# Performance work log

Hardware: AMD Instinct MI355X
Metric: run time of the kernel (lower is better)

Reference implementation:

```python
import jax, jax.numpy as jnp
import numpy as np

N = 20000      # num nodes
E = 320000     # num edges (before self loops)
DIN = 128      # in_channels
DH = 128       # hidden channels
C = 40         # num classes


def setup_inputs() -> dict:
    key = jax.random.key(0)
    ks = jax.random.split(key, 16)
    s_in = 1.0 / np.sqrt(DIN)
    s_h = 1.0 / np.sqrt(DH)
    s_a = 1.0 / np.sqrt(2 * DH)
    return {
        "x": jax.random.normal(ks[0], (N, DIN), jnp.float32),
        "edge_index": jax.random.randint(ks[1], (2, E), 0, N),
        "norm": jax.random.uniform(ks[2], (E + N,), jnp.float32),  # Jaccard sims in [0,1]
        # layer 1 params
        "W1": jax.random.uniform(ks[3], (DIN, DH), jnp.float32, -s_in, s_in),
        "aW1": jax.random.uniform(ks[4], (2 * DH, 1), jnp.float32, -s_a, s_a),
        "ab1": jax.random.uniform(ks[5], (1,), jnp.float32, -s_a, s_a),
        "alpha1": jnp.array([0.5], jnp.float32),
        "b1": jnp.zeros((DH,), jnp.float32),
        # layer 2 params
        "W2": jax.random.uniform(ks[6], (DH, DH), jnp.float32, -s_h, s_h),
        "aW2": jax.random.uniform(ks[7], (2 * DH, 1), jnp.float32, -s_a, s_a),
        "ab2": jax.random.uniform(ks[8], (1,), jnp.float32, -s_a, s_a),
        "alpha2": jnp.array([0.5], jnp.float32),
        "b2": jnp.zeros((DH,), jnp.float32),
        # output head
        "Wout": jax.random.uniform(ks[9], (DH, C), jnp.float32, -s_h, s_h),
        "bout": jax.random.uniform(ks[10], (C,), jnp.float32, -s_h, s_h),
    }


def _gat_layer(x, src, dst, norm, W, aW, ab, alpha, bias):
    n = x.shape[0]
    h = x @ W                              # [N, DH]
    s = h[src]                             # gathered source feats [E', DH]
    t = h[dst]                             # gathered target feats [E', DH]
    # attention logit per edge -> exp(leaky_relu(.))
    e = jnp.exp(jax.nn.leaky_relu(jnp.concatenate([s, t], axis=-1) @ aW + ab,
                                  negative_slope=0.2))          # [E', 1]
    e_sum = jax.ops.segment_sum(e, dst, num_segments=n)         # softmax denom per dst node
    a = e / e_sum[dst]
    s_sim = jnp.exp(norm)[:, None]                               # [E', 1]
    s_sum = jax.ops.segment_sum(s_sim, src, num_segments=n)     # note: summed over SRC (as in original)
    sw = s_sim / s_sum[dst]                                      # but indexed by DST (as in original)
    al = jnp.clip(alpha, 1e-4, 0.9999)
    w = al * a + (1.0 - al) * sw                                 # blended edge weight [E', 1]
    out = jax.ops.segment_max(w * s, dst, num_segments=n)        # aggr='max' propagate
    return out + bias


def reference(x, edge_index, norm, W1, aW1, ab1, alpha1, b1,
              W2, aW2, ab2, alpha2, b2, Wout, bout):
    n = x.shape[0]
    loops = jnp.arange(n, dtype=edge_index.dtype)
    src = jnp.concatenate([edge_index[0], loops])   # add_self_loops
    dst = jnp.concatenate([edge_index[1], loops])
    h = jax.nn.relu(_gat_layer(x, src, dst, norm, W1, aW1, ab1, alpha1, b1))
    h = jax.nn.relu(_gat_layer(h, src, dst, norm, W2, aW2, ab2, alpha2, b2))
    return jax.nn.log_softmax(h @ Wout + bout, axis=-1)
```

## Files before the change

kernel.cpp:

```cpp
#include <hip/hip_runtime.h>
#include <math.h>

#define DHID 128
#define NCLS 40
#define ELLW 64

typedef unsigned int   u32;
typedef unsigned short u16;
using short8 = __attribute__((ext_vector_type(8))) short;
using f32x4  = __attribute__((ext_vector_type(4))) float;

__device__ __forceinline__ u16 f2bf(float f) {
  u32 u = __float_as_uint(f);
  return (u16)((u + 0x7FFFu + ((u >> 16) & 1u)) >> 16);
}
__device__ __forceinline__ float bf_lo(u32 p) { return __uint_as_float(p << 16); }
__device__ __forceinline__ float bf_hi(u32 p) { return __uint_as_float(p & 0xFFFF0000u); }

__global__ __launch_bounds__(256) void prep_kernel(
    const float* __restrict__ x, const float* __restrict__ W1,
    const float* __restrict__ W2, u16* __restrict__ xbf,
    u16* __restrict__ Wp1, u16* __restrict__ Wp2,
    int* __restrict__ counts, float* __restrict__ ssum,
    int* __restrict__ ovf_cnt, int N) {
  int gi = blockIdx.x * 256 + threadIdx.x;
  int Ncvt = N * 16;
  if (gi < Ncvt) {
    int base = gi * 8;
    float4 v0 = *reinterpret_cast<const float4*>(x + base);
    float4 v1 = *reinterpret_cast<const float4*>(x + base + 4);
    uint4 o;
    o.x = (u32)f2bf(v0.x) | ((u32)f2bf(v0.y) << 16);
    o.y = (u32)f2bf(v0.z) | ((u32)f2bf(v0.w) << 16);
    o.z = (u32)f2bf(v1.x) | ((u32)f2bf(v1.y) << 16);
    o.w = (u32)f2bf(v1.z) | ((u32)f2bf(v1.w) << 16);
    *reinterpret_cast<uint4*>(xbf + base) = o;
    return;
  }
  gi -= Ncvt;
  if (gi < N) { counts[gi] = 0; ssum[gi] = 0.f; return; }
  gi -= N;
  if (gi < 32768) {
    int layer = gi >> 14, q = gi & 16383;
    int j = q & 7, l = (q >> 3) & 63, kt = (q >> 9) & 3, ct = q >> 11;
    int k = kt * 32 + (l >> 4) * 8 + j;
    int col = ct * 16 + (l & 15);
    const float* Wsrc = layer ? W2 : W1;
    u16* Wdst = layer ? Wp2 : Wp1;
    Wdst[q] = f2bf(Wsrc[k * DHID + col]);
    return;
  }
  gi -= 32768;
  if (gi == 0) *ovf_cnt = 0;
}

__device__ __forceinline__ void mfma_gemm_block(
    float* Cl, float* P, const u16* __restrict__ Xbf,
    const u16* __restrict__ Wp, const float* __restrict__ aW,
    u16* __restrict__ Hout, float* __restrict__ elo, float* __restrict__ ero,
    int n, int rowBase) {
  int t = threadIdx.x;
  int w = t >> 6, l = t & 63;
  int lr = l & 15, lh = l >> 4;
  f32x4 acc00 = {0.f,0.f,0.f,0.f}, acc01 = {0.f,0.f,0.f,0.f};
  f32x4 acc10 = {0.f,0.f,0.f,0.f}, acc11 = {0.f,0.f,0.f,0.f};
  int r0 = rowBase + lr;      if (r0 > n - 1) r0 = n - 1;
  int r1 = rowBase + 16 + lr; if (r1 > n - 1) r1 = n - 1;
  const u16* a0p = Xbf + (size_t)r0 * DHID;
  const u16* a1p = Xbf + (size_t)r1 * DHID;
  const u16* wb0 = Wp + ((size_t)(w * 2 + 0) * 4 * 64 + l) * 8;
  const u16* wb1 = Wp + ((size_t)(w * 2 + 1) * 4 * 64 + l) * 8;
#pragma unroll
  for (int kt = 0; kt < 4; ++kt) {
    int ko = kt * 32 + lh * 8;
    short8 fa0 = *reinterpret_cast<const short8*>(a0p + ko);
    short8 fa1 = *reinterpret_cast<const short8*>(a1p + ko);
    short8 fb0 = *reinterpret_cast<const short8*>(wb0 + kt * 64 * 8);
    short8 fb1 = *reinterpret_cast<const short8*>(wb1 + kt * 64 * 8);
    acc00 = __builtin_amdgcn_mfma_f32_16x16x32_bf16(fa0, fb0, acc00, 0, 0, 0);
    acc01 = __builtin_amdgcn_mfma_f32_16x16x32_bf16(fa0, fb1, acc01, 0, 0, 0);
    acc10 = __builtin_amdgcn_mfma_f32_16x16x32_bf16(fa1, fb0, acc10, 0, 0, 0);
    acc11 = __builtin_amdgcn_mfma_f32_16x16x32_bf16(fa1, fb1, acc11, 0, 0, 0);
  }
#pragma unroll
  for (int j = 0; j < 4; ++j) {
    Cl[(lh * 4 + j) * DHID + w * 32 + lr]           = acc00[j];
    Cl[(lh * 4 + j) * DHID + w * 32 + 16 + lr]      = acc01[j];
    Cl[(16 + lh * 4 + j) * DHID + w * 32 + lr]      = acc10[j];
    Cl[(16 + lh * 4 + j) * DHID + w * 32 + 16 + lr] = acc11[j];
  }
  __syncthreads();
  int r = t >> 3, cg2 = (t & 7) * 16;
  const float* crow = Cl + r * DHID + cg2;
  float pl = 0.f, pr = 0.f;
  int gr = rowBase + r;
#pragma unroll
  for (int q = 0; q < 16; ++q) {
    float v = crow[q];
    pl = fmaf(v, aW[cg2 + q], pl);
    pr = fmaf(v, aW[DHID + cg2 + q], pr);
  }
  if (gr < n) {
    uint4 o;
    o.x = (u32)f2bf(crow[0])  | ((u32)f2bf(crow[1])  << 16);
    o.y = (u32)f2bf(crow[2])  | ((u32)f2bf(crow[3])  << 16);
    o.z = (u32)f2bf(crow[4])  | ((u32)f2bf(crow[5])  << 16);
    o.w = (u32)f2bf(crow[6])  | ((u32)f2bf(crow[7])  << 16);
    *reinterpret_cast<uint4*>(Hout + (size_t)gr * DHID + cg2) = o;
    uint4 o2;
    o2.x = (u32)f2bf(crow[8])  | ((u32)f2bf(crow[9])  << 16);
    o2.y = (u32)f2bf(crow[10]) | ((u32)f2bf(crow[11]) << 16);
    o2.z = (u32)f2bf(crow[12]) | ((u32)f2bf(crow[13]) << 16);
    o2.w = (u32)f2bf(crow[14]) | ((u32)f2bf(crow[15]) << 16);
    *reinterpret_cast<uint4*>(Hout + (size_t)gr * DHID + cg2 + 8) = o2;
  }
  P[r * 16 + (t & 7) * 2 + 0] = pl;
  P[r * 16 + (t & 7) * 2 + 1] = pr;
  __syncthreads();
  if (t < 64) {
    int half = t >> 5, rr = t & 31;
    float s = 0.f;
#pragma unroll
    for (int cq = 0; cq < 8; ++cq) s += P[rr * 16 + cq * 2 + half];
    int g2 = rowBase + rr;
    if (g2 < n) { if (half) ero[g2] = s; else elo[g2] = s; }
  }
}

__global__ __launch_bounds__(256) void gemm1_build_kernel(
    const u16* __restrict__ Xbf, const u16* __restrict__ Wp,
    const float* __restrict__ aW, u16* __restrict__ H,
    float* __restrict__ el, float* __restrict__ er, int n, int gT,
    const int* __restrict__ ei, const float* __restrict__ norm,
    int* __restrict__ counts, float* __restrict__ ssum,
    uint2* __restrict__ ell, uint4* __restrict__ ovf,
    int* __restrict__ ovf_cnt, int E, int EP) {
  __shared__ float Cl[32 * DHID];
  __shared__ float P[32 * 16];
  if (blockIdx.x < gT) {
    mfma_gemm_block(Cl, P, Xbf, Wp, aW, H, el, er, n, blockIdx.x * 32);
  } else {
    int k = (blockIdx.x - gT) * 256 + threadIdx.x;
    if (k < EP) {
      int src, dst;
      if (k < E) { src = ei[k]; dst = ei[E + k]; }
      else       { src = dst = k - E; }
      float se = __expf(norm[k]);
      atomicAdd(&ssum[src], se);
      int slot = atomicAdd(&counts[dst], 1);
      if (slot < ELLW) {
        ell[(size_t)dst * ELLW + slot] =
            make_uint2((u32)src, __float_as_uint(se));
      } else {
        int o = atomicAdd(ovf_cnt, 1);
        ovf[o] = make_uint4((u32)dst, (u32)src, __float_as_uint(se), 0u);
      }
    }
  }
}

__global__ __launch_bounds__(256) void gemm_elr_kernel(
    const u16* __restrict__ Xbf, const u16* __restrict__ Wp,
    const float* __restrict__ aW, u16* __restrict__ H,
    float* __restrict__ el, float* __restrict__ er, int n) {
  __shared__ float Cl[32 * DHID];
  __shared__ float P[32 * 16];
  mfma_gemm_block(Cl, P, Xbf, Wp, aW, H, el, er, n, blockIdx.x * 32);
}

__device__ __forceinline__ void agg_node8(
    const u16* __restrict__ H, const int* __restrict__ counts,
    const uint2* __restrict__ ell, const uint4* __restrict__ ovf, int ovfN,
    const float* __restrict__ el, const float* __restrict__ ssum,
    float base, float al, int node, int lane, float a[8]) {
  int deg = counts[node];
  int dell = deg < ELLW ? deg : ELLW;
  const uint2* erow = ell + (size_t)node * ELLW;
  int src0 = 0; float sx0 = 0.f;
  if (lane < dell) {
    uint2 rec = erow[lane];
    src0 = (int)rec.x;
    sx0  = __uint_as_float(rec.y);
  }
  int qw = lane >> 4;
  const u16* Hf = H + ((lane & 15) << 3);
  int ei0 = qw, ei1 = 4 + qw;
  int ci0 = ei0 < dell ? ei0 : 0;
  int ci1 = ei1 < dell ? ei1 : 0;
  int ps0 = __shfl(src0, ci0);
  int ps1 = __shfl(src0, ci1);
  uint4 pr0 = *reinterpret_cast<const uint4*>(Hf + (size_t)ps0 * DHID);
  uint4 pr1 = *reinterpret_cast<const uint4*>(Hf + (size_t)ps1 * DHID);
  float e0 = 0.f;
  if (lane < dell) {
    float g = el[src0] + base;
    e0 = __expf(g > 0.f ? g : 0.2f * g);
  }
  float es = e0;
  if (ovfN > 0 && deg > ELLW) {
    for (int cb = 0; cb < ovfN; cb += 64) {
      int i = cb + lane;
      if (i < ovfN) {
        uint4 r = ovf[i];
        if ((int)r.x == node) {
          float g = el[(int)r.y] + base;
          es += __expf(g > 0.f ? g : 0.2f * g);
        }
      }
    }
  }
#pragma unroll
  for (int off = 32; off; off >>= 1) es += __shfl_xor(es, off);
  float invEs = al / es;
  float omaS  = (1.f - al) / ssum[node];
  float w0 = e0 * invEs + sx0 * omaS;
#pragma unroll
  for (int i = 0; i < 8; ++i) a[i] = -INFINITY;
  {
    float wA = __shfl(w0, ci0);
    float wB = __shfl(w0, ci1);
    if (ei0 < dell) {
      a[0] = fmaxf(a[0], wA * bf_lo(pr0.x)); a[1] = fmaxf(a[1], wA * bf_hi(pr0.x));
      a[2] = fmaxf(a[2], wA * bf_lo(pr0.y)); a[3] = fmaxf(a[3], wA * bf_hi(pr0.y));
      a[4] = fmaxf(a[4], wA * bf_lo(pr0.z)); a[5] = fmaxf(a[5], wA * bf_hi(pr0.z));
      a[6] = fmaxf(a[6], wA * bf_lo(pr0.w)); a[7] = fmaxf(a[7], wA * bf_hi(pr0.w));
    }
    if (ei1 < dell) {
      a[0] = fmaxf(a[0], wB * bf_lo(pr1.x)); a[1] = fmaxf(a[1], wB * bf_hi(pr1.x));
      a[2] = fmaxf(a[2], wB * bf_lo(pr1.y)); a[3] = fmaxf(a[3], wB * bf_hi(pr1.y));
      a[4] = fmaxf(a[4], wB * bf_lo(pr1.z)); a[5] = fmaxf(a[5], wB * bf_hi(pr1.z));
      a[6] = fmaxf(a[6], wB * bf_lo(pr1.w)); a[7] = fmaxf(a[7], wB * bf_hi(pr1.w));
    }
  }
  int j = 8;
  for (; j + 7 < dell; j += 8) {
    int ea = j + qw, eb = j + 4 + qw;
    int   sa = __shfl(src0, ea); float wa = __shfl(w0, ea);
    int   sb = __shfl(src0, eb); float wb = __shfl(w0, eb);
    uint4 ha = *reinterpret_cast<const uint4*>(Hf + (size_t)sa * DHID);
    uint4 hb = *reinterpret_cast<const uint4*>(Hf + (size_t)sb * DHID);
    a[0] = fmaxf(a[0], fmaxf(wa * bf_lo(ha.x), wb * bf_lo(hb.x)));
    a[1] = fmaxf(a[1], fmaxf(wa * bf_hi(ha.x), wb * bf_hi(hb.x)));
    a[2] = fmaxf(a[2], fmaxf(wa * bf_lo(ha.y), wb * bf_lo(hb.y)));
    a[3] = fmaxf(a[3], fmaxf(wa * bf_hi(ha.y), wb * bf_hi(hb.y)));
    a[4] = fmaxf(a[4], fmaxf(wa * bf_lo(ha.z), wb * bf_lo(hb.z)));
    a[5] = fmaxf(a[5], fmaxf(wa * bf_hi(ha.z), wb * bf_hi(hb.z)));
    a[6] = fmaxf(a[6], fmaxf(wa * bf_lo(ha.w), wb * bf_lo(hb.w)));
    a[7] = fmaxf(a[7], fmaxf(wa * bf_hi(ha.w), wb * bf_hi(hb.w)));
  }
  for (; j < dell; j += 4) {
    int e = j + qw;
    int ec = e < dell ? e : dell - 1;
    int   sa = __shfl(src0, ec); float wa = __shfl(w0, ec);
    if (e < dell) {
      uint4 ha = *reinterpret_cast<const uint4*>(Hf + (size_t)sa * DHID);
      a[0] = fmaxf(a[0], wa * bf_lo(ha.x));
      a[1] = fmaxf(a[1], wa * bf_hi(ha.x));
      a[2] = fmaxf(a[2], wa * bf_lo(ha.y));
      a[3] = fmaxf(a[3], wa * bf_hi(ha.y));
      a[4] = fmaxf(a[4], wa * bf_lo(ha.z));
      a[5] = fmaxf(a[5], wa * bf_hi(ha.z));
      a[6] = fmaxf(a[6], wa * bf_lo(ha.w));
      a[7] = fmaxf(a[7], wa * bf_hi(ha.w));
    }
  }
  if (ovfN > 0 && deg > ELLW) {
    for (int cb = 0; cb < ovfN; cb += 64) {
      int i = cb + lane;
      uint4 r = (i < ovfN) ? ovf[i] : make_uint4(0u, 0u, 0u, 0u);
      bool match = (i < ovfN) && ((int)r.x == node);
      int si = (int)r.y;
      float wi = 0.f;
      if (match) {
        float g = el[si] + base;
        wi = __expf(g > 0.f ? g : 0.2f * g) * invEs +
             __uint_as_float(r.z) * omaS;
      }
      unsigned long long mask = __ballot(match);
      while (mask) {
        int jb = __ffsll(mask) - 1;
        mask &= mask - 1;
        int   sj = __shfl(si, jb);
        float wj = __shfl(wi, jb);
        uint4 h = *reinterpret_cast<const uint4*>(Hf + (size_t)sj * DHID);
        a[0] = fmaxf(a[0], wj * bf_lo(h.x)); a[1] = fmaxf(a[1], wj * bf_hi(h.x));
        a[2] = fmaxf(a[2], wj * bf_lo(h.y)); a[3] = fmaxf(a[3], wj * bf_hi(h.y));
        a[4] = fmaxf(a[4], wj * bf_lo(h.z)); a[5] = fmaxf(a[5], wj * bf_hi(h.z));
        a[6] = fmaxf(a[6], wj * bf_lo(h.w)); a[7] = fmaxf(a[7], wj * bf_hi(h.w));
      }
    }
  }
#pragma unroll
  for (int i = 0; i < 8; ++i) {
    a[i] = fmaxf(a[i], __shfl_xor(a[i], 16));
    a[i] = fmaxf(a[i], __shfl_xor(a[i], 32));
  }
}

__global__ __launch_bounds__(256, 8) void agg_kernel(
    const u16* __restrict__ H, const int* __restrict__ counts,
    const uint2* __restrict__ ell, const uint4* __restrict__ ovf,
    const int* __restrict__ ovf_cnt, const float* __restrict__ el,
    const float* __restrict__ er, const float* __restrict__ ssum,
    const float* __restrict__ ab, const float* __restrict__ alpha,
    const float* __restrict__ bias, u16* __restrict__ Y, int n) {
  int node = blockIdx.x * 4 + (threadIdx.x >> 6);
  int lane = threadIdx.x & 63;
  if (node >= n) return;
  int ovfN = *ovf_cnt;
  float al = fminf(fmaxf(alpha[0], 1e-4f), 0.9999f);
  float base = er[node] + ab[0];
  float a[8];
  agg_node8(H, counts, ell, ovf, ovfN, el, ssum, base, al, node, lane, a);
  if (lane < 16) {
    int fl = lane << 3;
    float v[8];
#pragma unroll
    for (int i = 0; i < 8; ++i) v[i] = fmaxf(a[i] + bias[fl + i], 0.f);
    uint4 o;
    o.x = (u32)f2bf(v[0]) | ((u32)f2bf(v[1]) << 16);
    o.y = (u32)f2bf(v[2]) | ((u32)f2bf(v[3]) << 16);
    o.z = (u32)f2bf(v[4]) | ((u32)f2bf(v[5]) << 16);
    o.w = (u32)f2bf(v[6]) | ((u32)f2bf(v[7]) << 16);
    *reinterpret_cast<uint4*>(Y + (size_t)node * DHID + fl) = o;
  }
}

__global__ __launch_bounds__(256, 7) void agg_head_kernel(
    const u16* __restrict__ H, const int* __restrict__ counts,
    const uint2* __restrict__ ell, const uint4* __restrict__ ovf,
    const int* __restrict__ ovf_cnt, const float* __restrict__ el,
    const float* __restrict__ er, const float* __restrict__ ssum,
    const float* __restrict__ ab, const float* __restrict__ alpha,
    const float* __restrict__ bias, const float* __restrict__ Wout,
    const float* __restrict__ bout, float* __restrict__ out, int n) {
  __shared__ float Wl[DHID * NCLS];
  __shared__ float hl[4][DHID];
  int t = threadIdx.x;
  for (int i = t; i < DHID * NCLS; i += 256) Wl[i] = Wout[i];
  int wv = t >> 6, lane = t & 63;
  int node = blockIdx.x * 4 + wv;
  if (node < n) {
    int ovfN = *ovf_cnt;
    float al = fminf(fmaxf(alpha[0], 1e-4f), 0.9999f);
    float base = er[node] + ab[0];
    float a[8];
    agg_node8(H, counts, ell, ovf, ovfN, el, ssum, base, al, node, lane, a);
    if (lane < 16) {
      int fl = lane << 3;
#pragma unroll
      for (int i = 0; i < 8; ++i)
        hl[wv][fl + i] = fmaxf(a[i] + bias[fl + i], 0.f);
    }
  }
  __syncthreads();
  if (node >= n) return;
  float z = -INFINITY;
  bool act = lane < NCLS;
  if (act) {
    z = bout[lane];
    const float* hr = hl[wv];
#pragma unroll 8
    for (int k = 0; k < DHID; ++k) z = fmaf(hr[k], Wl[k * NCLS + lane], z);
  }
  float m = z;
#pragma unroll
  for (int off = 32; off; off >>= 1) m = fmaxf(m, __shfl_xor(m, off));
  float p = act ? expf(z - m) : 0.f;
#pragma unroll
  for (int off = 32; off; off >>= 1) p += __shfl_xor(p, off);
  float ls = logf(p);
  if (act) out[(size_t)node * NCLS + lane] = z - m - ls;
}

extern "C" void kernel_launch(void* const* d_in, const int* in_sizes, int n_in,
                              void* d_out, int out_size, void* d_ws, size_t ws_size,
                              hipStream_t stream) {
  const float* x     = (const float*)d_in[0];
  const int*   ei    = (const int*)d_in[1];
  const float* norm  = (const float*)d_in[2];
  const float* W1    = (const float*)d_in[3];
  const float* aW1   = (const float*)d_in[4];
  const float* ab1   = (const float*)d_in[5];
  const float* alpha1= (const float*)d_in[6];
  const float* b1    = (const float*)d_in[7];
  const float* W2    = (const float*)d_in[8];
  const float* aW2   = (const float*)d_in[9];
  const float* ab2   = (const float*)d_in[10];
  const float* alpha2= (const float*)d_in[11];
  const float* b2    = (const float*)d_in[12];
  const float* Wout  = (const float*)d_in[13];
  const float* bout  = (const float*)d_in[14];
  float* out = (float*)d_out;

  const int N  = in_sizes[0] / DHID;
  const int E  = in_sizes[1] / 2;
  const int EP = E + N;

  char* ws = (char*)d_ws;
  size_t off = 0;
  auto alloc = [&](size_t bytes) -> void* {
    void* p = ws + off;
    off += (bytes + 255) & ~(size_t)255;
    return p;
  };
  int*   counts  = (int*)  alloc((size_t)N * 4);
  float* ssum    = (float*)alloc((size_t)N * 4);
  int*   ovf_cnt = (int*)  alloc(256);
  u16*   xbf     = (u16*)  alloc((size_t)N * DHID * 2);
  u16*   Wp1     = (u16*)  alloc(16384 * 2);
  u16*   Wp2     = (u16*)  alloc(16384 * 2);
  u16*   Hbf     = (u16*)  alloc((size_t)N * DHID * 2);
  u16*   Bbf     = (u16*)  alloc((size_t)N * DHID * 2);
  float* el      = (float*)alloc((size_t)N * 4);
  float* er      = (float*)alloc((size_t)N * 4);
  uint2* ell     = (uint2*)alloc((size_t)N * ELLW * 8);
  uint4* ovf     = (uint4*)alloc((size_t)EP * 16);

  const int gEdge = (EP + 255) / 256;
  const int gT    = (N + 31) / 32;
  const int gAgg  = (N + 3) / 4;
  const int prepWork = N * 16 + N + 32768 + 1;
  const int gPrep = (prepWork + 255) / 256;

  prep_kernel<<<gPrep, 256, 0, stream>>>(x, W1, W2, xbf, Wp1, Wp2,
                                         counts, ssum, ovf_cnt, N);
  gemm1_build_kernel<<<gT + gEdge, 256, 0, stream>>>(
      xbf, Wp1, aW1, Hbf, el, er, N, gT, ei, norm, counts, ssum, ell, ovf,
      ovf_cnt, E, EP);
  agg_kernel<<<gAgg, 256, 0, stream>>>(Hbf, counts, ell, ovf, ovf_cnt, el, er,
                                       ssum, ab1, alpha1, b1, Bbf, N);
  gemm_elr_kernel<<<gT, 256, 0, stream>>>(Bbf, Wp2, aW2, Hbf, el, er, N);
  agg_head_kernel<<<gAgg, 256, 0, stream>>>(Hbf, counts, ell, ovf, ovf_cnt,
                                            el, er, ssum, ab2, alpha2, b2,
                                            Wout, bout, out, N);
}
```

Measured before the change: 105.0 us.

## Process two destination nodes per wavefront in aggregation kernels

```diff
diff --git a/kernel.cpp b/kernel.cpp
--- a/kernel.cpp
+++ b/kernel.cpp
@@ -16,6 +16,16 @@
 }
 __device__ __forceinline__ float bf_lo(u32 p) { return __uint_as_float(p << 16); }
 __device__ __forceinline__ float bf_hi(u32 p) { return __uint_as_float(p & 0xFFFF0000u); }
+
+#define FMAX8(acc, wv, h)                                            \
+  acc[0] = fmaxf(acc[0], (wv) * bf_lo((h).x));                       \
+  acc[1] = fmaxf(acc[1], (wv) * bf_hi((h).x));                       \
+  acc[2] = fmaxf(acc[2], (wv) * bf_lo((h).y));                       \
+  acc[3] = fmaxf(acc[3], (wv) * bf_hi((h).y));                       \
+  acc[4] = fmaxf(acc[4], (wv) * bf_lo((h).z));                       \
+  acc[5] = fmaxf(acc[5], (wv) * bf_hi((h).z));                       \
+  acc[6] = fmaxf(acc[6], (wv) * bf_lo((h).w));                       \
+  acc[7] = fmaxf(acc[7], (wv) * bf_hi((h).w));
 
 __global__ __launch_bounds__(256) void prep_kernel(
     const float* __restrict__ x, const float* __restrict__ W1,
@@ -168,165 +178,198 @@
   mfma_gemm_block(Cl, P, Xbf, Wp, aW, H, el, er, n, blockIdx.x * 32);
 }
 
-__device__ __forceinline__ void agg_node8(
+__device__ __forceinline__ void agg_node8_dual(
     const u16* __restrict__ H, const int* __restrict__ counts,
     const uint2* __restrict__ ell, const uint4* __restrict__ ovf, int ovfN,
-    const float* __restrict__ el, const float* __restrict__ ssum,
-    float base, float al, int node, int lane, float a[8]) {
-  int deg = counts[node];
-  int dell = deg < ELLW ? deg : ELLW;
-  const uint2* erow = ell + (size_t)node * ELLW;
-  int src0 = 0; float sx0 = 0.f;
-  if (lane < dell) {
-    uint2 rec = erow[lane];
-    src0 = (int)rec.x;
-    sx0  = __uint_as_float(rec.y);
-  }
+    const float* __restrict__ el, const float* __restrict__ er,
+    const float* __restrict__ ssum, float abv, float al,
+    int nodeA, int nodeB, int n, int lane, float aA[8], float aB[8]) {
+  int nB = nodeB < n ? nodeB : nodeA;
+  int degA = counts[nodeA], degB = counts[nB];
+  int dellA = degA < ELLW ? degA : ELLW;
+  int dellB = degB < ELLW ? degB : ELLW;
+  const uint2* erowA = ell + (size_t)nodeA * ELLW;
+  const uint2* erowB = ell + (size_t)nB * ELLW;
+  int srcA = 0, srcB = 0; float sxA = 0.f, sxB = 0.f;
+  if (lane < dellA) { uint2 r = erowA[lane]; srcA = (int)r.x; sxA = __uint_as_float(r.y); }
+  if (lane < dellB) { uint2 r = erowB[lane]; srcB = (int)r.x; sxB = __uint_as_float(r.y); }
   int qw = lane >> 4;
   const u16* Hf = H + ((lane & 15) << 3);
   int ei0 = qw, ei1 = 4 + qw;
-  int ci0 = ei0 < dell ? ei0 : 0;
-  int ci1 = ei1 < dell ? ei1 : 0;
-  int ps0 = __shfl(src0, ci0);
-  int ps1 = __shfl(src0, ci1);
-  uint4 pr0 = *reinterpret_cast<const uint4*>(Hf + (size_t)ps0 * DHID);
-  uint4 pr1 = *reinterpret_cast<const uint4*>(Hf + (size_t)ps1 * DHID);
-  float e0 = 0.f;
-  if (lane < dell) {
-    float g = el[src0] + base;
-    e0 = __expf(g > 0.f ? g : 0.2f * g);
-  }
-  float es = e0;
-  if (ovfN > 0 && deg > ELLW) {
+  int cA0 = ei0 < dellA ? ei0 : 0, cA1 = ei1 < dellA ? ei1 : 0;
+  int cB0 = ei0 < dellB ? ei0 : 0, cB1 = ei1 < dellB ? ei1 : 0;
+  int pA0 = __shfl(srcA, cA0), pA1 = __shfl(srcA, cA1);
+  int pB0 = __shfl(srcB, cB0), pB1 = __shfl(srcB, cB1);
+  uint4 rA0 = *reinterpret_cast<const uint4*>(Hf + (size_t)pA0 * DHID);
+  uint4 rA1 = *reinterpret_cast<const uint4*>(Hf + (size_t)pA1 * DHID);
+  uint4 rB0 = *reinterpret_cast<const uint4*>(Hf + (size_t)pB0 * DHID);
+  uint4 rB1 = *reinterpret_cast<const uint4*>(Hf + (size_t)pB1 * DHID);
+  float baseA = er[nodeA] + abv, baseB = er[nB] + abv;
+  float eA = 0.f, eB = 0.f;
+  if (lane < dellA) { float g = el[srcA] + baseA; eA = __expf(g > 0.f ? g : 0.2f * g); }
+  if (lane < dellB) { float g = el[srcB] + baseB; eB = __expf(g > 0.f ? g : 0.2f * g); }
+  float esA = eA, esB = eB;
+  if (ovfN > 0 && (degA > ELLW || degB > ELLW)) {
     for (int cb = 0; cb < ovfN; cb += 64) {
       int i = cb + lane;
       if (i < ovfN) {
         uint4 r = ovf[i];
-        if ((int)r.x == node) {
-          float g = el[(int)r.y] + base;
-          es += __expf(g > 0.f ? g : 0.2f * g);
-        }
-      }
-    }
-  }
-#pragma unroll
-  for (int off = 32; off; off >>= 1) es += __shfl_xor(es, off);
-  float invEs = al / es;
-  float omaS  = (1.f - al) / ssum[node];
-  float w0 = e0 * invEs + sx0 * omaS;
-#pragma unroll
-  for (int i = 0; i < 8; ++i) a[i] = -INFINITY;
+        if ((int)r.x == nodeA) { float g = el[(int)r.y] + baseA; esA += __expf(g > 0.f ? g : 0.2f * g); }
+        if ((int)r.x == nB)    { float g = el[(int)r.y] + baseB; esB += __expf(g > 0.f ? g : 0.2f * g); }
+      }
+    }
+  }
+#pragma unroll
+  for (int off = 32; off; off >>= 1) {
+    esA += __shfl_xor(esA, off);
+    esB += __shfl_xor(esB, off);
+  }
+  float invA = al / esA, invB = al / esB;
+  float omA = (1.f - al) / ssum[nodeA], omB = (1.f - al) / ssum[nB];
+  float w0A = eA * invA + sxA * omA;
+  float w0B = eB * invB + sxB * omB;
+#pragma unroll
+  for (int i = 0; i < 8; ++i) { aA[i] = -INFINITY; aB[i] = -INFINITY; }
   {
-    float wA = __shfl(w0, ci0);
-    float wB = __shfl(w0, ci1);
-    if (ei0 < dell) {
-      a[0] = fmaxf(a[0], wA * bf_lo(pr0.x)); a[1] = fmaxf(a[1], wA * bf_hi(pr0.x));
-      a[2] = fmaxf(a[2], wA * bf_lo(pr0.y)); a[3] = fmaxf(a[3], wA * bf_hi(pr0.y));
-      a[4] = fmaxf(a[4], wA * bf_lo(pr0.z)); a[5] = fmaxf(a[5], wA * bf_hi(pr0.z));
-      a[6] = fmaxf(a[6], wA * bf_lo(pr0.w)); a[7] = fmaxf(a[7], wA * bf_hi(pr0.w));
-    }
-    if (ei1 < dell) {
-      a[0] = fmaxf(a[0], wB * bf_lo(pr1.x)); a[1] = fmaxf(a[1], wB * bf_hi(pr1.x));
-      a[2] = fmaxf(a[2], wB * bf_lo(pr1.y)); a[3] = fmaxf(a[3], wB * bf_hi(pr1.y));
-      a[4] = fmaxf(a[4], wB * bf_lo(pr1.z)); a[5] = fmaxf(a[5], wB * bf_hi(pr1.z));
-      a[6] = fmaxf(a[6], wB * bf_lo(pr1.w)); a[7] = fmaxf(a[7], wB * bf_hi(pr1.w));
-    }
+    float wa = __shfl(w0A, cA0), wb = __shfl(w0A, cA1);
+    float wc = __shfl(w0B, cB0), wd = __shfl(w0B, cB1);
+    if (ei0 < dellA) { FMAX8(aA, wa, rA0) }
+    if (ei1 < dellA) { FMAX8(aA, wb, rA1) }
+    if (ei0 < dellB) { FMAX8(aB, wc, rB0) }
+    if (ei1 < dellB) { FMAX8(aB, wd, rB1) }
   }
   int j = 8;
-  for (; j + 7 < dell; j += 8) {
+  int dmin = dellA < dellB ? dellA : dellB;
+  for (; j + 7 < dmin; j += 8) {
     int ea = j + qw, eb = j + 4 + qw;
-    int   sa = __shfl(src0, ea); float wa = __shfl(w0, ea);
-    int   sb = __shfl(src0, eb); float wb = __shfl(w0, eb);
+    int sa = __shfl(srcA, ea); float wa = __shfl(w0A, ea);
+    int sb = __shfl(srcA, eb); float wb = __shfl(w0A, eb);
+    int sc = __shfl(srcB, ea); float wc = __shfl(w0B, ea);
+    int sd = __shfl(srcB, eb); float wd = __shfl(w0B, eb);
     uint4 ha = *reinterpret_cast<const uint4*>(Hf + (size_t)sa * DHID);
     uint4 hb = *reinterpret_cast<const uint4*>(Hf + (size_t)sb * DHID);
-    a[0] = fmaxf(a[0], fmaxf(wa * bf_lo(ha.x), wb * bf_lo(hb.x)));
-    a[1] = fmaxf(a[1], fmaxf(wa * bf_hi(ha.x), wb * bf_hi(hb.x)));
-    a[2] = fmaxf(a[2], fmaxf(wa * bf_lo(ha.y), wb * bf_lo(hb.y)));
-    a[3] = fmaxf(a[3], fmaxf(wa * bf_hi(ha.y), wb * bf_hi(hb.y)));
-    a[4] = fmaxf(a[4], fmaxf(wa * bf_lo(ha.z), wb * bf_lo(hb.z)));
-    a[5] = fmaxf(a[5], fmaxf(wa * bf_hi(ha.z), wb * bf_hi(hb.z)));
-    a[6] = fmaxf(a[6], fmaxf(wa * bf_lo(ha.w), wb * bf_lo(hb.w)));
-    a[7] = fmaxf(a[7], fmaxf(wa * bf_hi(ha.w), wb * bf_hi(hb.w)));
-  }
-  for (; j < dell; j += 4) {
-    int e = j + qw;
-    int ec = e < dell ? e : dell - 1;
-    int   sa = __shfl(src0, ec); float wa = __shfl(w0, ec);
-    if (e < dell) {
+    uint4 hc = *reinterpret_cast<const uint4*>(Hf + (size_t)sc * DHID);
+    uint4 hd = *reinterpret_cast<const uint4*>(Hf + (size_t)sd * DHID);
+    FMAX8(aA, wa, ha) FMAX8(aA, wb, hb)
+    FMAX8(aB, wc, hc) FMAX8(aB, wd, hd)
+  }
+  int jA = j, jB = j;
+  for (; jA + 7 < dellA; jA += 8) {
+    int ea = jA + qw, eb = jA + 4 + qw;
+    int sa = __shfl(srcA, ea); float wa = __shfl(w0A, ea);
+    int sb = __shfl(srcA, eb); float wb = __shfl(w0A, eb);
+    uint4 ha = *reinterpret_cast<const uint4*>(Hf + (size_t)sa * DHID);
+    uint4 hb = *reinterpret_cast<const uint4*>(Hf + (size_t)sb * DHID);
+    FMAX8(aA, wa, ha) FMAX8(aA, wb, hb)
+  }
+  for (; jA < dellA; jA += 4) {
+    int e = jA + qw;
+    int ec = e < dellA ? e : dellA - 1;
+    int sa = __shfl(srcA, ec); float wa = __shfl(w0A, ec);
+    if (e < dellA) {
       uint4 ha = *reinterpret_cast<const uint4*>(Hf + (size_t)sa * DHID);
-      a[0] = fmaxf(a[0], wa * bf_lo(ha.x));
-      a[1] = fmaxf(a[1], wa * bf_hi(ha.x));
-      a[2] = fmaxf(a[2], wa * bf_lo(ha.y));
-      a[3] = fmaxf(a[3], wa * bf_hi(ha.y));
-      a[4] = fmaxf(a[4], wa * bf_lo(ha.z));
-      a[5] = fmaxf(a[5], wa * bf_hi(ha.z));
-      a[6] = fmaxf(a[6], wa * bf_lo(ha.w));
-      a[7] = fmaxf(a[7], wa * bf_hi(ha.w));
-    }
-  }
-  if (ovfN > 0 && deg > ELLW) {
+      FMAX8(aA, wa, ha)
+    }
+  }
+  for (; jB + 7 < dellB; jB += 8) {
+    int ea = jB + qw, eb = jB + 4 + qw;
+    int sa = __shfl(srcB, ea); float wa = __shfl(w0B, ea);
+    int sb = __shfl(srcB, eb); float wb = __shfl(w0B, eb);
+    uint4 ha = *reinterpret_cast<const uint4*>(Hf + (size_t)sa * DHID);
+    uint4 hb = *reinterpret_cast<const uint4*>(Hf + (size_t)sb * DHID);
+    FMAX8(aB, wa, ha) FMAX8(aB, wb, hb)
+  }
+  for (; jB < dellB; jB += 4) {
+    int e = jB + qw;
+    int ec = e < dellB ? e : dellB - 1;
+    int sa = __shfl(srcB, ec); float wa = __shfl(w0B, ec);
+    if (e < dellB) {
+      uint4 ha = *reinterpret_cast<const uint4*>(Hf + (size_t)sa * DHID);
+      FMAX8(aB, wa, ha)
+    }
+  }
+  if (ovfN > 0 && (degA > ELLW || degB > ELLW)) {
     for (int cb = 0; cb < ovfN; cb += 64) {
       int i = cb + lane;
       uint4 r = (i < ovfN) ? ovf[i] : make_uint4(0u, 0u, 0u, 0u);
-      bool match = (i < ovfN) && ((int)r.x == node);
+      bool mA = (i < ovfN) && ((int)r.x == nodeA);
+      bool mB = (i < ovfN) && ((int)r.x == nB);
       int si = (int)r.y;
-      float wi = 0.f;
-      if (match) {
-        float g = el[si] + base;
-        wi = __expf(g > 0.f ? g : 0.2f * g) * invEs +
-             __uint_as_float(r.z) * omaS;
-      }
-      unsigned long long mask = __ballot(match);
+      float wiA = 0.f, wiB = 0.f;
+      if (mA) {
+        float g = el[si] + baseA;
+        wiA = __expf(g > 0.f ? g : 0.2f * g) * invA + __uint_as_float(r.z) * omA;
+      }
+      if (mB) {
+        float g = el[si] + baseB;
+        wiB = __expf(g > 0.f ? g : 0.2f * g) * invB + __uint_as_float(r.z) * omB;
+      }
+      unsigned long long mask = __ballot(mA);
       while (mask) {
-        int jb = __ffsll(mask) - 1;
-        mask &= mask - 1;
-        int   sj = __shfl(si, jb);
-        float wj = __shfl(wi, jb);
+        int jb = __ffsll(mask) - 1; mask &= mask - 1;
+        int sj = __shfl(si, jb); float wj = __shfl(wiA, jb);
         uint4 h = *reinterpret_cast<const uint4*>(Hf + (size_t)sj * DHID);
-        a[0] = fmaxf(a[0], wj * bf_lo(h.x)); a[1] = fmaxf(a[1], wj * bf_hi(h.x));
-        a[2] = fmaxf(a[2], wj * bf_lo(h.y)); a[3] = fmaxf(a[3], wj * bf_hi(h.y));
-        a[4] = fmaxf(a[4], wj * bf_lo(h.z)); a[5] = fmaxf(a[5], wj * bf_hi(h.z));
-        a[6] = fmaxf(a[6], wj * bf_lo(h.w)); a[7] = fmaxf(a[7], wj * bf_hi(h.w));
+        FMAX8(aA, wj, h)
+      }
+      mask = __ballot(mB);
+      while (mask) {
+        int jb = __ffsll(mask) - 1; mask &= mask - 1;
+        int sj = __shfl(si, jb); float wj = __shfl(wiB, jb);
+        uint4 h = *reinterpret_cast<const uint4*>(Hf + (size_t)sj * DHID);
+        FMAX8(aB, wj, h)
       }
     }
   }
 #pragma unroll
   for (int i = 0; i < 8; ++i) {
-    a[i] = fmaxf(a[i], __shfl_xor(a[i], 16));
-    a[i] = fmaxf(a[i], __shfl_xor(a[i], 32));
-  }
-}
-
-__global__ __launch_bounds__(256, 8) void agg_kernel(
+    aA[i] = fmaxf(aA[i], __shfl_xor(aA[i], 16));
+    aA[i] = fmaxf(aA[i], __shfl_xor(aA[i], 32));
+    aB[i] = fmaxf(aB[i], __shfl_xor(aB[i], 16));
+    aB[i] = fmaxf(aB[i], __shfl_xor(aB[i], 32));
+  }
+}
+
+__global__ __launch_bounds__(256) void agg_kernel(
     const u16* __restrict__ H, const int* __restrict__ counts,
     const uint2* __restrict__ ell, const uint4* __restrict__ ovf,
     const int* __restrict__ ovf_cnt, const float* __restrict__ el,
     const float* __restrict__ er, const float* __restrict__ ssum,
     const float* __restrict__ ab, const float* __restrict__ alpha,
     const float* __restrict__ bias, u16* __restrict__ Y, int n) {
-  int node = blockIdx.x * 4 + (threadIdx.x >> 6);
-  int lane = threadIdx.x & 63;
-  if (node >= n) return;
+  int wv = threadIdx.x >> 6, lane = threadIdx.x & 63;
+  int nodeA = blockIdx.x * 8 + wv * 2;
+  int nodeB = nodeA + 1;
+  if (nodeA >= n) return;
   int ovfN = *ovf_cnt;
   float al = fminf(fmaxf(alpha[0], 1e-4f), 0.9999f);
-  float base = er[node] + ab[0];
-  float a[8];
-  agg_node8(H, counts, ell, ovf, ovfN, el, ssum, base, al, node, lane, a);
+  float aA[8], aB[8];
+  agg_node8_dual(H, counts, ell, ovf, ovfN, el, er, ssum, ab[0], al,
+                 nodeA, nodeB, n, lane, aA, aB);
   if (lane < 16) {
     int fl = lane << 3;
     float v[8];
 #pragma unroll
-    for (int i = 0; i < 8; ++i) v[i] = fmaxf(a[i] + bias[fl + i], 0.f);
+    for (int i = 0; i < 8; ++i) v[i] = fmaxf(aA[i] + bias[fl + i], 0.f);
     uint4 o;
     o.x = (u32)f2bf(v[0]) | ((u32)f2bf(v[1]) << 16);
     o.y = (u32)f2bf(v[2]) | ((u32)f2bf(v[3]) << 16);
     o.z = (u32)f2bf(v[4]) | ((u32)f2bf(v[5]) << 16);
     o.w = (u32)f2bf(v[6]) | ((u32)f2bf(v[7]) << 16);
-    *reinterpret_cast<uint4*>(Y + (size_t)node * DHID + fl) = o;
-  }
-}
-
-__global__ __launch_bounds__(256, 7) void agg_head_kernel(
+    *reinterpret_cast<uint4*>(Y + (size_t)nodeA * DHID + fl) = o;
+    if (nodeB < n) {
+#pragma unroll
+      for (int i = 0; i < 8; ++i) v[i] = fmaxf(aB[i] + bias[fl + i], 0.f);
+      uint4 o2;
+      o2.x = (u32)f2bf(v[0]) | ((u32)f2bf(v[1]) << 16);
+      o2.y = (u32)f2bf(v[2]) | ((u32)f2bf(v[3]) << 16);
+      o2.z = (u32)f2bf(v[4]) | ((u32)f2bf(v[5]) << 16);
+      o2.w = (u32)f2bf(v[6]) | ((u32)f2bf(v[7]) << 16);
+      *reinterpret_cast<uint4*>(Y + (size_t)nodeB * DHID + fl) = o2;
+    }
+  }
+}
+
+__global__ __launch_bounds__(256) void agg_head_kernel(
     const u16* __restrict__ H, const int* __restrict__ counts,
     const uint2* __restrict__ ell, const uint4* __restrict__ ovf,
     const int* __restrict__ ovf_cnt, const float* __restrict__ el,
@@ -335,42 +378,50 @@
     const float* __restrict__ bias, const float* __restrict__ Wout,
     const float* __restrict__ bout, float* __restrict__ out, int n) {
   __shared__ float Wl[DHID * NCLS];
-  __shared__ float hl[4][DHID];
+  __shared__ float hl[8][DHID];
   int t = threadIdx.x;
   for (int i = t; i < DHID * NCLS; i += 256) Wl[i] = Wout[i];
   int wv = t >> 6, lane = t & 63;
-  int node = blockIdx.x * 4 + wv;
-  if (node < n) {
+  int nodeA = blockIdx.x * 8 + wv * 2;
+  int nodeB = nodeA + 1;
+  if (nodeA < n) {
     int ovfN = *ovf_cnt;
     float al = fminf(fmaxf(alpha[0], 1e-4f), 0.9999f);
-    float base = er[node] + ab[0];
-    float a[8];
-    agg_node8(H, counts, ell, ovf, ovfN, el, ssum, base, al, node, lane, a);
+    float aA[8], aB[8];
+    agg_node8_dual(H, counts, ell, ovf, ovfN, el, er, ssum, ab[0], al,
+                   nodeA, nodeB, n, lane, aA, aB);
     if (lane < 16) {
       int fl = lane << 3;
 #pragma unroll
       for (int i = 0; i < 8; ++i)
-        hl[wv][fl + i] = fmaxf(a[i] + bias[fl + i], 0.f);
+        hl[wv * 2][fl + i] = fmaxf(aA[i] + bias[fl + i], 0.f);
+#pragma unroll
+      for (int i = 0; i < 8; ++i)
+        hl[wv * 2 + 1][fl + i] = fmaxf(aB[i] + bias[fl + i], 0.f);
     }
   }
   __syncthreads();
-  if (node >= n) return;
-  float z = -INFINITY;
-  bool act = lane < NCLS;
-  if (act) {
-    z = bout[lane];
-    const float* hr = hl[wv];
+#pragma unroll 1
+  for (int q = 0; q < 2; ++q) {
+    int node = nodeA + q;
+    if (node >= n) continue;
+    float z = -INFINITY;
+    bool act = lane < NCLS;
+    if (act) {
+      z = bout[lane];
+      const float* hr = hl[wv * 2 + q];
 #pragma unroll 8
-    for (int k = 0; k < DHID; ++k) z = fmaf(hr[k], Wl[k * NCLS + lane], z);
-  }
-  float m = z;
-#pragma unroll
-  for (int off = 32; off; off >>= 1) m = fmaxf(m, __shfl_xor(m, off));
-  float p = act ? expf(z - m) : 0.f;
-#pragma unroll
-  for (int off = 32; off; off >>= 1) p += __shfl_xor(p, off);
-  float ls = logf(p);
-  if (act) out[(size_t)node * NCLS + lane] = z - m - ls;
+      for (int k = 0; k < DHID; ++k) z = fmaf(hr[k], Wl[k * NCLS + lane], z);
+    }
+    float m = z;
+#pragma unroll
+    for (int off = 32; off; off >>= 1) m = fmaxf(m, __shfl_xor(m, off));
+    float p = act ? expf(z - m) : 0.f;
+#pragma unroll
+    for (int off = 32; off; off >>= 1) p += __shfl_xor(p, off);
+    float ls = logf(p);
+    if (act) out[(size_t)node * NCLS + lane] = z - m - ls;
+  }
 }
 
 extern "C" void kernel_launch(void* const* d_in, const int* in_sizes, int n_in,
@@ -419,7 +470,7 @@
 
   const int gEdge = (EP + 255) / 256;
   const int gT    = (N + 31) / 32;
-  const int gAgg  = (N + 3) / 4;
+  const int gAgg  = (N + 7) / 8;
   const int prepWork = N * 16 + N + 32768 + 1;
   const int gPrep = (prepWork + 255) / 256;
 
```

Measured after the change: 109.0 us. 1.04x slower.
